# Kernel optimization log

Measured on AMD Instinct MI355X. Metric: run time of the kernel, lower is better.

Reference implementation:

```python
import jax, jax.numpy as jnp
import numpy as np

THRESHOLD = 0.5
ALPHA = 1.0
N, D = 100000, 256
B, K = 1024, 128


def _l2norm(x):
    # F.normalize(x, p=2, dim=-1) with eps=1e-12
    return x / jnp.maximum(jnp.linalg.norm(x, axis=-1, keepdims=True), 1e-12)


def setup_inputs() -> dict:
    key = jax.random.key(0)
    k1, k2, k3, k4, k5, k6, k7 = jax.random.split(key, 7)
    feature = jax.random.normal(k1, (N, D), dtype=jnp.float32)
    text_embedding = jax.random.normal(k2, (N, D), dtype=jnp.float32)
    virtual = jax.random.normal(k3, (1, D), dtype=jnp.float32)
    # Gumbel(0,1) noise for gumbel_softmax (tau=1), materialized for determinism
    u = jax.random.uniform(k4, (B, K, K), dtype=jnp.float32, minval=1e-6, maxval=1.0 - 1e-6)
    gumbel = -jnp.log(-jnp.log(u))
    ego_nodes = jnp.sort(jax.random.randint(k5, (B, K), 0, N, dtype=jnp.int32), axis=-1)
    edges_adj = jax.random.randint(k6, (B, K, K), 0, 2, dtype=jnp.int32)
    train_label = jax.random.randint(k7, (B,), 0, 2, dtype=jnp.int32)
    return {"feature": feature, "text_embedding": text_embedding, "virtual": virtual,
            "gumbel": gumbel, "ego_nodes": ego_nodes, "edges_adj": edges_adj,
            "train_label": train_label}


def reference(feature, text_embedding, virtual, gumbel, ego_nodes, edges_adj, train_label):
    feat = _l2norm(feature)          # self.feature (normalized in __init__)
    emb = _l2norm(text_embedding)    # self.embedding
    te_local = _l2norm(emb - virtual)            # [N, D]

    tb = te_local[ego_nodes]                     # [B, K, D] gather per ego-subgraph
    sim = jnp.einsum('bkd,bjd->bkj', tb, tb) - THRESHOLD   # [B, K, K]
    sim_sub = jax.nn.softmax(sim + gumbel, axis=-1)         # gumbel_softmax, tau=1

    adj = edges_adj.astype(sim_sub.dtype)        # scatter edges_adj[src,dst]=1, precomputed
    # s_diff: row-wise L2 norm then mean over rows
    s_diff = jnp.sqrt(jnp.sum((adj - sim_sub) ** 2, axis=-1)).mean(axis=-1)   # [B]

    emb_out = feat[ego_nodes].mean(axis=1)       # [B, D] sum(feature)/n
    emb_pg = emb[ego_nodes].mean(axis=1)         # [B, D] sum(embedding)/n  (n == K)
    f_diff = jnp.linalg.norm(emb_out - emb_pg, axis=-1)                        # [B]

    score = s_diff + ALPHA * f_diff
    score = (score - score.min()) / (score.max() - score.min())

    y = train_label.astype(score.dtype)
    eps = 1e-7  # stabilizes log at exact 0/1 (torch BCELoss clamps log at -100)
    sc = jnp.clip(score, eps, 1.0 - eps)
    bce = -(y * jnp.log(sc) + (1.0 - y) * jnp.log1p(-sc)).mean()
    loss = bce / y.shape[0]
    return score, loss
```

## Files before the change

### kernel.cpp

```cpp
#include <hip/hip_runtime.h>
#include <hip/hip_bf16.h>
#include <math.h>

#define DIM 256
#define BB 1024
#define KK 128
#define PITCH 264

typedef __attribute__((ext_vector_type(8))) short short8;
typedef __attribute__((ext_vector_type(4))) float float4v;

__device__ __forceinline__ float dot4(const float4 a, const float4 b) {
    return a.x*b.x + a.y*b.y + a.z*b.z + a.w*b.w;
}

__device__ __forceinline__ unsigned bf2bits(float a, float b) {
    float2 t; t.x = a; t.y = b;
    __hip_bfloat162 h = __float22bfloat162_rn(t);
    unsigned u; __builtin_memcpy(&u, &h, 4);
    return u;
}

__global__ __attribute__((amdgpu_flat_work_group_size(1024, 1024),
                          amdgpu_waves_per_eu(8, 8)))
void fused_main(
    const float* __restrict__ feature,
    const float* __restrict__ text,
    const float* __restrict__ virt,
    const float* __restrict__ gumbel,
    const int*   __restrict__ ego,
    const int*   __restrict__ adj,
    float*       __restrict__ score_raw)
{
    __shared__ unsigned short tbs[KK * PITCH];
    __shared__ float fpart8[8][DIM];
    __shared__ float rowpart[KK][8];
    __shared__ float spart[2];

    const int b    = blockIdx.x;
    const int tid  = threadIdx.x;
    const int wave = tid >> 6;
    const int lane = tid & 63;

    const int* ego_b = ego + b * KK;

    const float4 vm = ((const float4*)virt)[lane];
    float vv2 = dot4(vm, vm);
    #pragma unroll
    for (int m = 1; m < 64; m <<= 1) vv2 += __shfl_xor(vv2, m);

    const int baseA = wave * 8;
    int eidx[8];
    #pragma unroll
    for (int k = 0; k < 8; ++k) eidx[k] = ego_b[baseA + k];

    float4 fdv = make_float4(0.f, 0.f, 0.f, 0.f);

    float4 pt[2], pf[2];
    #pragma unroll
    for (int p = 0; p < 2; ++p) {
        pt[p] = ((const float4*)(text    + (size_t)eidx[p] * DIM))[lane];
        pf[p] = ((const float4*)(feature + (size_t)eidx[p] * DIM))[lane];
    }

    #pragma unroll
    for (int k = 0; k < 8; ++k) {
        const int sl = k & 1;
        const float4 ct = pt[sl], cf = pf[sl];
        if (k < 6) {
            pt[sl] = ((const float4*)(text    + (size_t)eidx[k+2] * DIM))[lane];
            pf[sl] = ((const float4*)(feature + (size_t)eidx[k+2] * DIM))[lane];
        }

        float st = dot4(ct, ct), sf = dot4(cf, cf), sv = dot4(ct, vm);
        #pragma unroll
        for (int m = 1; m < 64; m <<= 1) {
            st += __shfl_xor(st, m);
            sf += __shfl_xor(sf, m);
            sv += __shfl_xor(sv, m);
        }

        const float inv_ne = __builtin_amdgcn_rsqf(fmaxf(st, 1e-24f));
        const float inv_nf = __builtin_amdgcn_rsqf(fmaxf(sf, 1e-24f));
        const float nw2    = fmaxf(1.f + vv2 - 2.f * sv * inv_ne, 1e-24f);
        const float inv_nt = __builtin_amdgcn_rsqf(nw2);

        const float e0 = ct.x * inv_ne, e1 = ct.y * inv_ne;
        const float e2 = ct.z * inv_ne, e3 = ct.w * inv_ne;
        fdv.x += cf.x * inv_nf - e0;
        fdv.y += cf.y * inv_nf - e1;
        fdv.z += cf.z * inv_nf - e2;
        fdv.w += cf.w * inv_nf - e3;

        uint2 pk;
        pk.x = bf2bits((e0 - vm.x) * inv_nt, (e1 - vm.y) * inv_nt);
        pk.y = bf2bits((e2 - vm.z) * inv_nt, (e3 - vm.w) * inv_nt);
        *(uint2*)&tbs[(baseA + k) * PITCH + 4 * lane] = pk;
    }

    if (wave & 1) *(float4*)&fpart8[wave >> 1][4 * lane] = fdv;

    __syncthreads();

    if (!(wave & 1)) {
        float4 o = *(float4*)&fpart8[wave >> 1][4 * lane];
        o.x += fdv.x; o.y += fdv.y; o.z += fdv.z; o.w += fdv.w;
        *(float4*)&fpart8[wave >> 1][4 * lane] = o;
    }

    const int strip = wave >> 1;
    const int half  = wave & 1;
    const int g     = lane >> 4;
    const int c     = lane & 15;
    const int baseR = strip * 16;

    const float* gr = gumbel + ((size_t)b * KK + baseR + g*4) * KK + half*64 + c;
    const int*   ar = adj    + ((size_t)b * KK + baseR + g*4) * KK + half*64 + c;

    float4v acc[4];
    const float4v zero = {0.f, 0.f, 0.f, 0.f};
    #pragma unroll
    for (int t = 0; t < 4; ++t) acc[t] = zero;

    int   atmp[16];
    float gvv[16];

    #pragma unroll
    for (int q = 0; q < 8; ++q) {
        if (q < 4) {
            #pragma unroll
            for (int t = 0; t < 4; ++t)
                atmp[q*4 + t] = __builtin_nontemporal_load(ar + q*KK + t*16);
        } else {
            const int r = q - 4;
            #pragma unroll
            for (int t = 0; t < 4; ++t)
                gvv[r*4 + t] = __builtin_nontemporal_load(gr + r*KK + t*16);
        }
        const int dq = q * 32 + g * 8;
        const short8 afr = *(const short8*)&tbs[(baseR + c) * PITCH + dq];
        #pragma unroll
        for (int t = 0; t < 4; ++t) {
            const short8 bfr = *(const short8*)&tbs[(half*64 + t*16 + c) * PITCH + dq];
            acc[t] = __builtin_amdgcn_mfma_f32_16x16x32_bf16(afr, bfr, acc[t], 0, 0, 0);
        }
    }

    #pragma unroll
    for (int r = 0; r < 4; ++r) {
        float s = 0.f, a2 = 0.f, a3 = 0.f;
        int   ia = 0;
        #pragma unroll
        for (int t = 0; t < 4; ++t) {
            const float vt = acc[t][r] - 0.5f + gvv[r*4 + t];
            const float et = __expf(vt);
            const int   ad = atmp[r*4 + t];
            s  += et;
            a3 += et * et;
            a2 += ad ? et : 0.f;
            ia += ad ? 1 : 0;
        }
        float fia = (float)ia;
        #pragma unroll
        for (int msk = 1; msk < 16; msk <<= 1) {
            s   += __shfl_xor(s,   msk);
            a2  += __shfl_xor(a2,  msk);
            a3  += __shfl_xor(a3,  msk);
            fia += __shfl_xor(fia, msk);
        }
        if (c == 0) {
            float4 pk4; pk4.x = s; pk4.y = a2; pk4.z = a3; pk4.w = fia;
            *(float4*)&rowpart[baseR + g*4 + r][half * 4] = pk4;
        }
    }

    __syncthreads();

    if (tid < KK) {
        const float4 pa = *(const float4*)&rowpart[tid][0];
        const float4 pb = *(const float4*)&rowpart[tid][4];
        const float s   = pa.x + pb.x;
        const float a2  = pa.y + pb.y;
        const float a3  = pa.z + pb.z;
        const float fia = pa.w + pb.w;
        const float invS = __builtin_amdgcn_rcpf(s);
        float sq = sqrtf(fmaxf(fia - invS * (2.f * a2 - invS * a3), 0.f));
        #pragma unroll
        for (int m = 1; m < 64; m <<= 1) sq += __shfl_xor(sq, m);
        if (lane == 0) spart[wave] = sq;
    }

    __syncthreads();

    if (wave == 0) {
        float4 d = make_float4(0.f, 0.f, 0.f, 0.f);
        #pragma unroll
        for (int j = 0; j < 8; ++j) {
            const float4 p = *(const float4*)&fpart8[j][4 * lane];
            d.x += p.x; d.y += p.y; d.z += p.z; d.w += p.w;
        }
        const float inv = 1.f / 128.f;
        d.x *= inv; d.y *= inv; d.z *= inv; d.w *= inv;
        float q2 = dot4(d, d);
        #pragma unroll
        for (int m = 1; m < 64; m <<= 1) q2 += __shfl_xor(q2, m);
        if (lane == 0)
            score_raw[b] = (spart[0] + spart[1]) * (1.f / 128.f) + sqrtf(q2);
    }
}

__global__ __launch_bounds__(1024) void finalize(
    const float* __restrict__ score_raw,
    const int*   __restrict__ label,
    float*       __restrict__ out)
{
    __shared__ float wmin[16], wmax[16], wsum[16];
    const int tid = threadIdx.x;
    const float s = score_raw[tid];
    float mn = s, mx = s;
    #pragma unroll
    for (int m = 1; m < 64; m <<= 1) {
        mn = fminf(mn, __shfl_xor(mn, m));
        mx = fmaxf(mx, __shfl_xor(mx, m));
    }
    if ((tid & 63) == 0) { wmin[tid >> 6] = mn; wmax[tid >> 6] = mx; }
    __syncthreads();
    float gmn = wmin[0], gmx = wmax[0];
    #pragma unroll
    for (int w = 1; w < 16; ++w) {
        gmn = fminf(gmn, wmin[w]);
        gmx = fmaxf(gmx, wmax[w]);
    }
    const float score = (s - gmn) / (gmx - gmn);
    out[tid] = score;

    const float y  = (float)label[tid];
    const float sc = fminf(fmaxf(score, 1e-7f), 1.f - 1e-7f);
    float term = -(y * logf(sc) + (1.f - y) * log1pf(-sc));
    #pragma unroll
    for (int m = 1; m < 64; m <<= 1) term += __shfl_xor(term, m);
    if ((tid & 63) == 0) wsum[tid >> 6] = term;
    __syncthreads();
    if (tid == 0) {
        float tot = 0.f;
        #pragma unroll
        for (int w = 0; w < 16; ++w) tot += wsum[w];
        out[BB] = tot / (1024.f * 1024.f);
    }
}

extern "C" void kernel_launch(void* const* d_in, const int* in_sizes, int n_in,
                              void* d_out, int out_size, void* d_ws, size_t ws_size,
                              hipStream_t stream) {
    const float* feature = (const float*)d_in[0];
    const float* text    = (const float*)d_in[1];
    const float* virt    = (const float*)d_in[2];
    const float* gumbel  = (const float*)d_in[3];
    const int*   ego     = (const int*)d_in[4];
    const int*   adj     = (const int*)d_in[5];
    const int*   label   = (const int*)d_in[6];
    float* out       = (float*)d_out;
    float* score_raw = (float*)d_ws;

    fused_main<<<BB, 1024, 0, stream>>>(feature, text, virt, gumbel, ego, adj, score_raw);
    finalize<<<1, 1024, 0, stream>>>(score_raw, label, out);
}
```

Baseline: 74.80 us.

## Halve block size, give each wave 16 rows, use DPP row reductions

After: 70.11 us. 6.3% less time.

```diff
diff --git a/kernel.cpp b/kernel.cpp
--- a/kernel.cpp
+++ b/kernel.cpp
@@ -21,9 +21,26 @@
     return u;
 }
 
-__global__ __attribute__((amdgpu_flat_work_group_size(1024, 1024),
-                          amdgpu_waves_per_eu(8, 8)))
-void fused_main(
+template<int CTRL>
+__device__ __forceinline__ float addror(float x) {
+    int r = __builtin_amdgcn_update_dpp(0, __float_as_int(x), CTRL, 0xF, 0xF, true);
+    return x + __int_as_float(r);
+}
+__device__ __forceinline__ float sum16dpp(float x) {
+    x = addror<0x121>(x);
+    x = addror<0x122>(x);
+    x = addror<0x124>(x);
+    x = addror<0x128>(x);
+    return x;
+}
+__device__ __forceinline__ float sum64dpp(float x) {
+    x = sum16dpp(x);
+    x += __shfl_xor(x, 16);
+    x += __shfl_xor(x, 32);
+    return x;
+}
+
+__global__ __launch_bounds__(512, 4) void fused_main(
     const float* __restrict__ feature,
     const float* __restrict__ text,
     const float* __restrict__ virt,
@@ -33,7 +50,7 @@
     float*       __restrict__ score_raw)
 {
     __shared__ unsigned short tbs[KK * PITCH];
-    __shared__ float fpart8[8][DIM];
+    __shared__ float fpart[8][DIM];
     __shared__ float rowpart[KK][8];
     __shared__ float spart[2];
 
@@ -42,135 +59,118 @@
     const int wave = tid >> 6;
     const int lane = tid & 63;
 
+    const float4 vm = ((const float4*)virt)[lane];
+    const float vv2 = sum64dpp(dot4(vm, vm));
+
     const int* ego_b = ego + b * KK;
-
-    const float4 vm = ((const float4*)virt)[lane];
-    float vv2 = dot4(vm, vm);
-    #pragma unroll
-    for (int m = 1; m < 64; m <<= 1) vv2 += __shfl_xor(vv2, m);
-
-    const int baseA = wave * 8;
-    int eidx[8];
-    #pragma unroll
-    for (int k = 0; k < 8; ++k) eidx[k] = ego_b[baseA + k];
+    const int  base  = wave * 16;
 
     float4 fdv = make_float4(0.f, 0.f, 0.f, 0.f);
 
-    float4 pt[2], pf[2];
-    #pragma unroll
-    for (int p = 0; p < 2; ++p) {
-        pt[p] = ((const float4*)(text    + (size_t)eidx[p] * DIM))[lane];
-        pf[p] = ((const float4*)(feature + (size_t)eidx[p] * DIM))[lane];
-    }
-
-    #pragma unroll
-    for (int k = 0; k < 8; ++k) {
-        const int sl = k & 1;
-        const float4 ct = pt[sl], cf = pf[sl];
-        if (k < 6) {
-            pt[sl] = ((const float4*)(text    + (size_t)eidx[k+2] * DIM))[lane];
-            pf[sl] = ((const float4*)(feature + (size_t)eidx[k+2] * DIM))[lane];
-        }
-
-        float st = dot4(ct, ct), sf = dot4(cf, cf), sv = dot4(ct, vm);
-        #pragma unroll
-        for (int m = 1; m < 64; m <<= 1) {
-            st += __shfl_xor(st, m);
-            sf += __shfl_xor(sf, m);
-            sv += __shfl_xor(sv, m);
-        }
-
-        const float inv_ne = __builtin_amdgcn_rsqf(fmaxf(st, 1e-24f));
-        const float inv_nf = __builtin_amdgcn_rsqf(fmaxf(sf, 1e-24f));
-        const float nw2    = fmaxf(1.f + vv2 - 2.f * sv * inv_ne, 1e-24f);
-        const float inv_nt = __builtin_amdgcn_rsqf(nw2);
-
-        const float e0 = ct.x * inv_ne, e1 = ct.y * inv_ne;
-        const float e2 = ct.z * inv_ne, e3 = ct.w * inv_ne;
-        fdv.x += cf.x * inv_nf - e0;
-        fdv.y += cf.y * inv_nf - e1;
-        fdv.z += cf.z * inv_nf - e2;
-        fdv.w += cf.w * inv_nf - e3;
-
-        uint2 pk;
-        pk.x = bf2bits((e0 - vm.x) * inv_nt, (e1 - vm.y) * inv_nt);
-        pk.y = bf2bits((e2 - vm.z) * inv_nt, (e3 - vm.w) * inv_nt);
-        *(uint2*)&tbs[(baseA + k) * PITCH + 4 * lane] = pk;
-    }
-
-    if (wave & 1) *(float4*)&fpart8[wave >> 1][4 * lane] = fdv;
-
-    __syncthreads();
-
-    if (!(wave & 1)) {
-        float4 o = *(float4*)&fpart8[wave >> 1][4 * lane];
-        o.x += fdv.x; o.y += fdv.y; o.z += fdv.z; o.w += fdv.w;
-        *(float4*)&fpart8[wave >> 1][4 * lane] = o;
-    }
-
-    const int strip = wave >> 1;
-    const int half  = wave & 1;
-    const int g     = lane >> 4;
-    const int c     = lane & 15;
-    const int baseR = strip * 16;
-
-    const float* gr = gumbel + ((size_t)b * KK + baseR + g*4) * KK + half*64 + c;
-    const int*   ar = adj    + ((size_t)b * KK + baseR + g*4) * KK + half*64 + c;
-
-    float4v acc[4];
-    const float4v zero = {0.f, 0.f, 0.f, 0.f};
-    #pragma unroll
-    for (int t = 0; t < 4; ++t) acc[t] = zero;
-
-    int   atmp[16];
-    float gvv[16];
-
-    #pragma unroll
-    for (int q = 0; q < 8; ++q) {
-        if (q < 4) {
+    #pragma unroll
+    for (int bt = 0; bt < 4; ++bt) {
+        const int r0 = base + bt * 4;
+        const int e0i = ego_b[r0 + 0], e1i = ego_b[r0 + 1];
+        const int e2i = ego_b[r0 + 2], e3i = ego_b[r0 + 3];
+        const float4 T0 = ((const float4*)(text + (size_t)e0i * DIM))[lane];
+        const float4 T1 = ((const float4*)(text + (size_t)e1i * DIM))[lane];
+        const float4 T2 = ((const float4*)(text + (size_t)e2i * DIM))[lane];
+        const float4 T3 = ((const float4*)(text + (size_t)e3i * DIM))[lane];
+        const float4 F0 = ((const float4*)(feature + (size_t)e0i * DIM))[lane];
+        const float4 F1 = ((const float4*)(feature + (size_t)e1i * DIM))[lane];
+        const float4 F2 = ((const float4*)(feature + (size_t)e2i * DIM))[lane];
+        const float4 F3 = ((const float4*)(feature + (size_t)e3i * DIM))[lane];
+
+        float st0 = dot4(T0, T0), sv0 = dot4(T0, vm), sf0 = dot4(F0, F0);
+        float st1 = dot4(T1, T1), sv1 = dot4(T1, vm), sf1 = dot4(F1, F1);
+        float st2 = dot4(T2, T2), sv2 = dot4(T2, vm), sf2 = dot4(F2, F2);
+        float st3 = dot4(T3, T3), sv3 = dot4(T3, vm), sf3 = dot4(F3, F3);
+
+        st0 = sum64dpp(st0); sv0 = sum64dpp(sv0); sf0 = sum64dpp(sf0);
+        st1 = sum64dpp(st1); sv1 = sum64dpp(sv1); sf1 = sum64dpp(sf1);
+        st2 = sum64dpp(st2); sv2 = sum64dpp(sv2); sf2 = sum64dpp(sf2);
+        st3 = sum64dpp(st3); sv3 = sum64dpp(sv3); sf3 = sum64dpp(sf3);
+
+        #define NORMROW(Tj, Fj, stj, sfj, svj, ROW)                              \
+        {                                                                        \
+            const float inv_ne = __builtin_amdgcn_rsqf(fmaxf(stj, 1e-24f));      \
+            const float inv_nf = __builtin_amdgcn_rsqf(fmaxf(sfj, 1e-24f));      \
+            const float nw2    = fmaxf(1.f + vv2 - 2.f * svj * inv_ne, 1e-24f);  \
+            const float inv_nt = __builtin_amdgcn_rsqf(nw2);                     \
+            const float e0 = Tj.x * inv_ne, e1 = Tj.y * inv_ne;                  \
+            const float e2 = Tj.z * inv_ne, e3 = Tj.w * inv_ne;                  \
+            fdv.x += Fj.x * inv_nf - e0;  fdv.y += Fj.y * inv_nf - e1;           \
+            fdv.z += Fj.z * inv_nf - e2;  fdv.w += Fj.w * inv_nf - e3;           \
+            uint2 pk;                                                            \
+            pk.x = bf2bits((e0 - vm.x) * inv_nt, (e1 - vm.y) * inv_nt);          \
+            pk.y = bf2bits((e2 - vm.z) * inv_nt, (e3 - vm.w) * inv_nt);          \
+            *(uint2*)&tbs[(ROW) * PITCH + 4 * lane] = pk;                        \
+        }
+        NORMROW(T0, F0, st0, sf0, sv0, r0 + 0)
+        NORMROW(T1, F1, st1, sf1, sv1, r0 + 1)
+        NORMROW(T2, F2, st2, sf2, sv2, r0 + 2)
+        NORMROW(T3, F3, st3, sf3, sv3, r0 + 3)
+        #undef NORMROW
+    }
+    *(float4*)&fpart[wave][4 * lane] = fdv;
+
+    __syncthreads();
+
+    const int g = lane >> 4;
+    const int c = lane & 15;
+
+    #pragma unroll
+    for (int h = 0; h < 2; ++h) {
+        float4v acc[4];
+        #pragma unroll
+        for (int t = 0; t < 4; ++t) acc[t] = (float4v){0.f, 0.f, 0.f, 0.f};
+
+        #pragma unroll
+        for (int q = 0; q < 8; ++q) {
+            const int dq = q * 32 + g * 8;
+            const short8 afr = *(const short8*)&tbs[(base + c) * PITCH + dq];
             #pragma unroll
-            for (int t = 0; t < 4; ++t)
-                atmp[q*4 + t] = __builtin_nontemporal_load(ar + q*KK + t*16);
-        } else {
-            const int r = q - 4;
-            #pragma unroll
-            for (int t = 0; t < 4; ++t)
-                gvv[r*4 + t] = __builtin_nontemporal_load(gr + r*KK + t*16);
-        }
-        const int dq = q * 32 + g * 8;
-        const short8 afr = *(const short8*)&tbs[(baseR + c) * PITCH + dq];
-        #pragma unroll
-        for (int t = 0; t < 4; ++t) {
-            const short8 bfr = *(const short8*)&tbs[(half*64 + t*16 + c) * PITCH + dq];
-            acc[t] = __builtin_amdgcn_mfma_f32_16x16x32_bf16(afr, bfr, acc[t], 0, 0, 0);
-        }
-    }
-
-    #pragma unroll
-    for (int r = 0; r < 4; ++r) {
-        float s = 0.f, a2 = 0.f, a3 = 0.f;
-        int   ia = 0;
-        #pragma unroll
-        for (int t = 0; t < 4; ++t) {
-            const float vt = acc[t][r] - 0.5f + gvv[r*4 + t];
-            const float et = __expf(vt);
-            const int   ad = atmp[r*4 + t];
-            s  += et;
-            a3 += et * et;
-            a2 += ad ? et : 0.f;
-            ia += ad ? 1 : 0;
-        }
-        float fia = (float)ia;
-        #pragma unroll
-        for (int msk = 1; msk < 16; msk <<= 1) {
-            s   += __shfl_xor(s,   msk);
-            a2  += __shfl_xor(a2,  msk);
-            a3  += __shfl_xor(a3,  msk);
-            fia += __shfl_xor(fia, msk);
-        }
-        if (c == 0) {
-            float4 pk4; pk4.x = s; pk4.y = a2; pk4.z = a3; pk4.w = fia;
-            *(float4*)&rowpart[baseR + g*4 + r][half * 4] = pk4;
+            for (int t = 0; t < 4; ++t) {
+                const short8 bfr = *(const short8*)&tbs[(h * 64 + t * 16 + c) * PITCH + dq];
+                acc[t] = __builtin_amdgcn_mfma_f32_16x16x32_bf16(afr, bfr, acc[t], 0, 0, 0);
+            }
+        }
+
+        const float* gr = gumbel + ((size_t)b * KK + base + g * 4) * KK + h * 64 + c;
+        const int*   ar = adj    + ((size_t)b * KK + base + g * 4) * KK + h * 64 + c;
+
+        #pragma unroll
+        for (int r = 0; r < 4; ++r) {
+            int av0 = __builtin_nontemporal_load(ar + r * KK);
+            int av1 = __builtin_nontemporal_load(ar + r * KK + 16);
+            int av2 = __builtin_nontemporal_load(ar + r * KK + 32);
+            int av3 = __builtin_nontemporal_load(ar + r * KK + 48);
+            float gv0 = __builtin_nontemporal_load(gr + r * KK);
+            float gv1 = __builtin_nontemporal_load(gr + r * KK + 16);
+            float gv2 = __builtin_nontemporal_load(gr + r * KK + 32);
+            float gv3 = __builtin_nontemporal_load(gr + r * KK + 48);
+
+            const float et0 = __expf(acc[0][r] - 0.5f + gv0);
+            const float et1 = __expf(acc[1][r] - 0.5f + gv1);
+            const float et2 = __expf(acc[2][r] - 0.5f + gv2);
+            const float et3 = __expf(acc[3][r] - 0.5f + gv3);
+
+            float s   = et0 + et1 + et2 + et3;
+            float a3  = et0*et0 + et1*et1 + et2*et2 + et3*et3;
+            float a2  = (av0 ? et0 : 0.f) + (av1 ? et1 : 0.f)
+                      + (av2 ? et2 : 0.f) + (av3 ? et3 : 0.f);
+            float fia = (av0 ? 1.f : 0.f) + (av1 ? 1.f : 0.f)
+                      + (av2 ? 1.f : 0.f) + (av3 ? 1.f : 0.f);
+
+            s   = sum16dpp(s);
+            a2  = sum16dpp(a2);
+            a3  = sum16dpp(a3);
+            fia = sum16dpp(fia);
+
+            if (c == 0) {
+                float4 pk4; pk4.x = s; pk4.y = a2; pk4.z = a3; pk4.w = fia;
+                *(float4*)&rowpart[base + g * 4 + r][h * 4] = pk4;
+            }
         }
     }
 
@@ -185,8 +185,7 @@
         const float fia = pa.w + pb.w;
         const float invS = __builtin_amdgcn_rcpf(s);
         float sq = sqrtf(fmaxf(fia - invS * (2.f * a2 - invS * a3), 0.f));
-        #pragma unroll
-        for (int m = 1; m < 64; m <<= 1) sq += __shfl_xor(sq, m);
+        sq = sum64dpp(sq);
         if (lane == 0) spart[wave] = sq;
     }
 
@@ -196,14 +195,12 @@
         float4 d = make_float4(0.f, 0.f, 0.f, 0.f);
         #pragma unroll
         for (int j = 0; j < 8; ++j) {
-            const float4 p = *(const float4*)&fpart8[j][4 * lane];
+            const float4 p = *(const float4*)&fpart[j][4 * lane];
             d.x += p.x; d.y += p.y; d.z += p.z; d.w += p.w;
         }
         const float inv = 1.f / 128.f;
         d.x *= inv; d.y *= inv; d.z *= inv; d.w *= inv;
-        float q2 = dot4(d, d);
-        #pragma unroll
-        for (int m = 1; m < 64; m <<= 1) q2 += __shfl_xor(q2, m);
+        const float q2 = sum64dpp(dot4(d, d));
         if (lane == 0)
             score_raw[b] = (spart[0] + spart[1]) * (1.f / 128.f) + sqrtf(q2);
     }
@@ -262,6 +259,6 @@
     float* out       = (float*)d_out;
     float* score_raw = (float*)d_ws;
 
-    fused_main<<<BB, 1024, 0, stream>>>(feature, text, virt, gumbel, ego, adj, score_raw);
+    fused_main<<<BB, 512, 0, stream>>>(feature, text, virt, gumbel, ego, adj, score_raw);
     finalize<<<1, 1024, 0, stream>>>(score_raw, label, out);
 }
```
